# Optimization experiments

Hardware: AMD Instinct MI355X
Metric: run time of the kernel (lower is better)

## Reference

```python
import jax, jax.numpy as jnp
import numpy as np

B, S, DM, H, DK, DV, CUT = 2, 256, 512, 8, 64, 64, 16
LN_EPS = 1e-5


def get_con_vecs(seq, cutoff):
    # seq: (B, H, S, d). Faithful to torch: raw row-major reshape, NOT a transpose.
    b, h, s, d = seq.shape
    D = h * d
    flat = seq.reshape(b, s, D)                       # raw reinterpretation as in torch
    t = jnp.broadcast_to(flat[:, None], (b, s, s, D)) # (B, S_rep, S_orig, D)
    t = t.transpose(0, 3, 1, 2)                       # (B, D, S, S)
    up = jnp.triu(t)
    up = jnp.flip(up, axis=2)
    up = jnp.pad(up, ((0, 0), (0, 0), (1, 0), (0, 0)))[:, :, :-1, :]
    low = jnp.tril(t)
    low = jnp.flip(low, axis=2)
    mtx = jnp.concatenate([up, low], axis=-1)         # (B, D, S, 2S)
    mtx = mtx.transpose(0, 2, 3, 1)                   # (B, S, 2S, D)
    mtx = mtx.reshape(b, h, s, 2 * s, d)              # raw reinterpretation as in torch
    c = min(cutoff, s)
    return mtx[:, :, :, s - c:s + c, :]               # (B, H, S, 2c, d)


def setup_inputs():
    key = jax.random.key(0)
    ks = jax.random.split(key, 14)
    n = lambda k, shp, sc=0.02: jax.random.normal(k, shp, dtype=jnp.float32) * sc
    return {
        "Q": jax.random.normal(ks[0], (B, S, DM), dtype=jnp.float32),
        "K": jax.random.normal(ks[1], (B, S, DM), dtype=jnp.float32),
        "V": jax.random.normal(ks[2], (B, S, DM), dtype=jnp.float32),
        "attn_mask": jax.random.randint(ks[3], (B, S, S), 0, 2).astype(bool),
        "WQ": n(ks[4], (DM, H * DK)), "bQ": jnp.zeros((H * DK,), jnp.float32),
        "WK": n(ks[5], (DM, H * DK)), "bK": jnp.zeros((H * DK,), jnp.float32),
        "WV": n(ks[6], (DM, H * DV)), "bV": jnp.zeros((H * DV,), jnp.float32),
        "Wo": n(ks[7], (H * DV, DM)), "bo": jnp.zeros((DM,), jnp.float32),
        "gamma": jnp.ones((DM,), jnp.float32), "beta": jnp.zeros((DM,), jnp.float32),
    }


def reference(Q, K, V, attn_mask, WQ, bQ, WK, bK, WV, bV, Wo, bo, gamma, beta):
    b = Q.shape[0]
    q_s = (Q @ WQ + bQ).reshape(b, -1, H, DK).transpose(0, 2, 1, 3)  # (B,H,S,dk)
    k_s = (K @ WK + bK).reshape(b, -1, H, DK).transpose(0, 2, 1, 3)
    v_s = (V @ WV + bV).reshape(b, -1, H, DV).transpose(0, 2, 1, 3)  # unused in 'con' path (V := con(K))
    del v_s

    Qc = get_con_vecs(q_s, CUT)   # (B,H,S,2c,dk)
    Kc = get_con_vecs(k_s, CUT)
    Vc = Kc

    scores = jnp.einsum('bhqcd,bhkcd->bhqkc', Qc, Kc) / np.float32(np.sqrt(DK))
    mask = attn_mask[:, None, :, :, None]             # (B,1,S,S,1) -> broadcast over heads, 2c
    scores = jnp.where(mask, jnp.float32(-1e9), scores)
    attn = jax.nn.softmax(scores, axis=-1)            # softmax over the 2c context axis
    context = jnp.einsum('bhqkc,bhvcd->bhqd', attn, Vc)
    attn_out = attn.sum(axis=-1)                      # (B,H,S,S)

    ctx = context.transpose(0, 2, 1, 3).reshape(b, -1, H * DV)
    out = ctx @ Wo + bo
    y = out + Q
    mu = y.mean(axis=-1, keepdims=True)
    var = ((y - mu) ** 2).mean(axis=-1, keepdims=True)
    y_n = (y - mu) / jnp.sqrt(var + LN_EPS) * gamma + beta
    return (y_n, attn_out)
```

## Files before the change

### kernel.cpp

```cpp
#include <hip/hip_runtime.h>

#define LN_EPS 1e-5f


#define FMA4(a, s, v) { (a).x += (s)*(v).x; (a).y += (s)*(v).y; \
                        (a).z += (s)*(v).z; (a).w += (s)*(v).w; }

__device__ __forceinline__ bool sniff_mask_bytes(const unsigned int* m) {
    unsigned int acc = 0;
#pragma unroll
    for (int i = 0; i < 16; ++i) acc |= m[i];
    return acc > 1u;
}

__global__ __launch_bounds__(512) void kAo_proj_part(
    const float* __restrict__ Qin, const float* __restrict__ Kin,
    const float* __restrict__ WQ, const float* __restrict__ WK,
    float* __restrict__ Ppart)
{
    __shared__ float Xs[32][36];
    int bx = blockIdx.x;
    int mc = bx & 15, b = (bx >> 4) & 1, which = bx >> 5;
    int m0 = mc * 32;
    int t = threadIdx.x;

    const float* In = which ? Kin : Qin;
    const float* W  = which ? WK  : WQ;

#pragma unroll
    for (int i = 0; i < 2; ++i) {
        int idx = i * 512 + t;
        int fr = idx >> 5, mm = idx & 31;
        int cc = fr >> 3, cs = fr & 7;
        int srow = (cc < 2) ? (240 + 8 * cc + cs) : (8 * (cc - 2) + cs);
        Xs[mm][fr] = In[(b * 256 + srow) * 512 + m0 + mm];
    }
    __syncthreads();

    int h_i = t >> 6, g = t >> 7;
    int cc0 = (h_i & 1) * 2;
    float acc[16];
#pragma unroll
    for (int j = 0; j < 16; ++j) acc[j] = 0.f;

    const float* wp = W + t;
#pragma unroll 4
    for (int mm = 0; mm < 32; ++mm) {
        float w = wp[(m0 + mm) * 512];
        const float4* xp = (const float4*)&Xs[mm][cc0 * 8];
        float4 x0 = xp[0], x1 = xp[1], x2 = xp[2], x3 = xp[3];
        acc[0]  += x0.x * w; acc[1]  += x0.y * w; acc[2]  += x0.z * w; acc[3]  += x0.w * w;
        acc[4]  += x1.x * w; acc[5]  += x1.y * w; acc[6]  += x1.z * w; acc[7]  += x1.w * w;
        acc[8]  += x2.x * w; acc[9]  += x2.y * w; acc[10] += x2.z * w; acc[11] += x2.w * w;
        acc[12] += x3.x * w; acc[13] += x3.y * w; acc[14] += x3.z * w; acc[15] += x3.w * w;
    }

    int d = t & 63;
    int base = ((which * 2 + b) * 4 + g) * 4;
#pragma unroll
    for (int j = 0; j < 16; ++j) {
        int ccj = cc0 + (j >> 3), cs = j & 7;
        Ppart[mc * 32768 + (base + ccj) * 512 + cs * 64 + d] = acc[j];
    }
}

__global__ void kB_proj_red(const float* __restrict__ Ppart,
                            const float* __restrict__ bQ, const float* __restrict__ bK,
                            float* __restrict__ F) {
    int f = blockIdx.x * 256 + threadIdx.x;
    float acc = 0.f;
#pragma unroll
    for (int kc = 0; kc < 16; ++kc) acc += Ppart[kc * 32768 + f];
    int which = f >> 14, cc = (f >> 9) & 3, g = (f >> 11) & 3, d = f & 63;
    int n = (g * 2 + (cc >> 1)) * 64 + d;
    F[f] = acc + (which ? bK[n] : bQ[n]);
}

__global__ void kC_dtab_sfk(const float* __restrict__ F, float* __restrict__ Dt,
                            float* __restrict__ SFK) {
    int slot = blockIdx.x * 256 + threadIdx.x;
    if (slot < 8192) {
        int part = slot & 7, e = slot >> 3;
        int cs = e & 7, cc = (e >> 3) & 3, gk = (e >> 5) & 3,
            gq = (e >> 7) & 3, b = (e >> 9) & 1;
        const float* fq = F + ((b * 4 + gq) * 4 + cc) * 512 + cs * 64 + part * 8;
        const float* fk = F + (((2 + b) * 4 + gk) * 4 + cc) * 512 + cs * 64 + part * 8;
        float a = 0.f;
#pragma unroll
        for (int u = 0; u < 8; ++u) a += fq[u] * fk[u];
        a += __shfl_xor(a, 1);
        a += __shfl_xor(a, 2);
        a += __shfl_xor(a, 4);
        if (part == 0) Dt[e] = a * 0.125f;
    } else {
        int e = slot - 8192;
        int d = e & 63, c = (e >> 6) & 31, b = e >> 11;
        float a = 0.f;
#pragma unroll
        for (int gv = 0; gv < 4; ++gv)
            a += F[(((2 + b) * 4 + gv) * 4 + (c >> 3)) * 512 + (c & 7) * 64 + d];
        SFK[e] = 32.f * a;
    }
}

__global__ void kAttn(const float* __restrict__ Dt, const void* __restrict__ maskp,
                      const float* __restrict__ SFK, float* __restrict__ ctx,
                      float* __restrict__ attnp, int fill) {
    __shared__ float aws[4][32];
    int vb = blockIdx.x, t = threadIdx.x;
    if (fill) ((float4*)attnp)[vb * 256 + t] = make_float4(1.f, 1.f, 1.f, 1.f);
    int qb = vb & 63, h = (vb >> 6) & 7, b = vb >> 9;
    int wave = t >> 6, l = t & 63;
    int q = qb * 4 + wave;
    int half = l & 1, klo = l >> 1;
    int g_q = q & 3;
    int i_q = h * 32 + (q >> 3);
    bool up_q = (q & 4) == 0;
    int ak = klo & 3;
    bool up_k = (klo & 4) == 0;

    bool mbytes = sniff_mask_bytes((const unsigned int*)maskp);

    float sq[16];
    const float* Db = Dt + ((b * 4 + g_q) * 4 + ak) * 32 + half * 16;
#pragma unroll
    for (int j = 0; j < 16; ++j) {
        int cc = half * 2 + (j >> 3);
        int row = g_q * 64 + 30 + cc;
        bool vq = up_q ? (i_q >= 256 - row) : (i_q <= 255 - row);
        sq[j] = vq ? Db[j] : 0.f;
    }

    float A[16];
#pragma unroll
    for (int j = 0; j < 16; ++j) A[j] = 0.f;

    int qrow = (b * 256 + q) * 256;
    for (int r = 0; r < 8; ++r) {
        int k = r * 32 + klo;
        bool masked = mbytes ? (((const unsigned char*)maskp)[qrow + k] != 0)
                             : (((const int*)maskp)[qrow + k] != 0);
        if (masked) {
#pragma unroll
            for (int j = 0; j < 16; ++j) A[j] += 0.03125f;
            continue;
        }
        int i_k = h * 32 + (k >> 3);
        float s[16];
        float mx = -1e30f;
#pragma unroll
        for (int j = 0; j < 16; ++j) {
            int cc = half * 2 + (j >> 3);
            int row = ak * 64 + 30 + cc;
            bool vk = up_k ? (i_k >= 256 - row) : (i_k <= 255 - row);
            s[j] = vk ? sq[j] : 0.f;
            mx = fmaxf(mx, s[j]);
        }
        mx = fmaxf(mx, __shfl_xor(mx, 1));
        float den = 0.f;
#pragma unroll
        for (int j = 0; j < 16; ++j) { s[j] = __expf(s[j] - mx); den += s[j]; }
        den += __shfl_xor(den, 1);
        float inv = 1.f / den;
#pragma unroll
        for (int j = 0; j < 16; ++j) A[j] += s[j] * inv;
    }

#pragma unroll
    for (int off = 2; off < 64; off <<= 1) {
#pragma unroll
        for (int j = 0; j < 16; ++j) A[j] += __shfl_xor(A[j], off);
    }

    float* aw = aws[wave];
    if (l < 2) {
#pragma unroll
        for (int j = 0; j < 16; ++j) aw[l * 16 + j] = A[j];
    }
    float acc = 0.f;
    const float* S = SFK + b * 2048;
#pragma unroll
    for (int c = 0; c < 32; ++c) acc += aw[c] * S[c * 64 + l];
    ctx[(b * 256 + q) * 512 + h * 64 + l] = acc;
}

__global__ __launch_bounds__(512) void kG4LN(
    const float* __restrict__ ctx, const float* __restrict__ Wo,
    const float* __restrict__ bo, const float* __restrict__ Qin,
    const float* __restrict__ gamma, const float* __restrict__ beta,
    float* __restrict__ out)
{
    __shared__ float  Cl[4][512];
    __shared__ float4 red4[8][4][64];
    __shared__ float  red2[8][2];

    int t = threadIdx.x, r0 = blockIdx.x * 4;
    int w = t >> 6, l = t & 63;

    ((float4*)Cl)[t] = ((const float4*)&ctx[r0 * 512])[t];
    __syncthreads();

    const float4* WoV = (const float4*)Wo;
    const float4* pA = WoV + (size_t)(w * 64) * 128 + l;
    const float4* pB = pA + 64;
    float4 a0A = {0,0,0,0}, a1A = {0,0,0,0}, a2A = {0,0,0,0}, a3A = {0,0,0,0};
    float4 a0B = {0,0,0,0}, a1B = {0,0,0,0}, a2B = {0,0,0,0}, a3B = {0,0,0,0};
    int m0 = w * 64;
    float4 wA = pA[0], wB = pB[0];
#pragma unroll 4
    for (int mm = 0; mm < 63; ++mm) {
        float4 nA = pA[(mm + 1) * 128];
        float4 nB = pB[(mm + 1) * 128];
        float s0 = Cl[0][m0 + mm], s1 = Cl[1][m0 + mm];
        float s2 = Cl[2][m0 + mm], s3 = Cl[3][m0 + mm];
        FMA4(a0A, s0, wA); FMA4(a1A, s1, wA); FMA4(a2A, s2, wA); FMA4(a3A, s3, wA);
        FMA4(a0B, s0, wB); FMA4(a1B, s1, wB); FMA4(a2B, s2, wB); FMA4(a3B, s3, wB);
        wA = nA; wB = nB;
    }
    {
        float s0 = Cl[0][m0 + 63], s1 = Cl[1][m0 + 63];
        float s2 = Cl[2][m0 + 63], s3 = Cl[3][m0 + 63];
        FMA4(a0A, s0, wA); FMA4(a1A, s1, wA); FMA4(a2A, s2, wA); FMA4(a3A, s3, wA);
        FMA4(a0B, s0, wB); FMA4(a1B, s1, wB); FMA4(a2B, s2, wB); FMA4(a3B, s3, wB);
    }

    red4[w][0][l] = a0A; red4[w][1][l] = a1A; red4[w][2][l] = a2A; red4[w][3][l] = a3A;
    __syncthreads();
    if (t < 256) {
        int r = t >> 6, c4 = t & 63;
        float4 s = red4[0][r][c4];
#pragma unroll
        for (int w2 = 1; w2 < 8; ++w2) {
            float4 v = red4[w2][r][c4];
            s.x += v.x; s.y += v.y; s.z += v.z; s.w += v.w;
        }
        float4 bb = ((const float4*)bo)[c4];
        float4 qq = ((const float4*)Qin)[(r0 + r) * 128 + c4];
        s.x += bb.x + qq.x; s.y += bb.y + qq.y;
        s.z += bb.z + qq.z; s.w += bb.w + qq.w;
        *(float4*)&Cl[r][c4 * 4] = s;
    }
    __syncthreads();
    red4[w][0][l] = a0B; red4[w][1][l] = a1B; red4[w][2][l] = a2B; red4[w][3][l] = a3B;
    __syncthreads();
    if (t < 256) {
        int r = t >> 6, c4 = t & 63;
        float4 s = red4[0][r][c4];
#pragma unroll
        for (int w2 = 1; w2 < 8; ++w2) {
            float4 v = red4[w2][r][c4];
            s.x += v.x; s.y += v.y; s.z += v.z; s.w += v.w;
        }
        float4 bb = ((const float4*)bo)[64 + c4];
        float4 qq = ((const float4*)Qin)[(r0 + r) * 128 + 64 + c4];
        s.x += bb.x + qq.x; s.y += bb.y + qq.y;
        s.z += bb.z + qq.z; s.w += bb.w + qq.w;
        *(float4*)&Cl[r][256 + c4 * 4] = s;
    }
    __syncthreads();

    int r = t >> 7, c = t & 127;
    float v0 = Cl[r][c], v1 = Cl[r][c + 128], v2 = Cl[r][c + 256], v3 = Cl[r][c + 384];
    float s1 = v0 + v1 + v2 + v3;
    float s2 = v0 * v0 + v1 * v1 + v2 * v2 + v3 * v3;
#pragma unroll
    for (int off = 1; off < 64; off <<= 1) {
        s1 += __shfl_xor(s1, off);
        s2 += __shfl_xor(s2, off);
    }
    if (l == 0) { red2[w][0] = s1; red2[w][1] = s2; }
    __syncthreads();
    float tot1 = red2[2 * r][0] + red2[2 * r + 1][0];
    float tot2 = red2[2 * r][1] + red2[2 * r + 1][1];
    float mu = tot1 * (1.f / 512.f);
    float var = tot2 * (1.f / 512.f) - mu * mu;
    float rs = rsqrtf(var + LN_EPS);
    float* op = out + (r0 + r) * 512;
    op[c]       = (v0 - mu) * rs * gamma[c]       + beta[c];
    op[c + 128] = (v1 - mu) * rs * gamma[c + 128] + beta[c + 128];
    op[c + 256] = (v2 - mu) * rs * gamma[c + 256] + beta[c + 256];
    op[c + 384] = (v3 - mu) * rs * gamma[c + 384] + beta[c + 384];
}

__global__ void k5_fill(float* __restrict__ p, int n) {
    int i = (blockIdx.x * 256 + threadIdx.x) * 4;
    float4 one = make_float4(1.f, 1.f, 1.f, 1.f);
    for (; i < n; i += gridDim.x * 256 * 4) *(float4*)(p + i) = one;
}

extern "C" void kernel_launch(void* const* d_in, const int* in_sizes, int n_in,
                              void* d_out, int out_size, void* d_ws, size_t ws_size,
                              hipStream_t stream) {
    (void)in_sizes; (void)n_in; (void)out_size;
    const float* Qin  = (const float*)d_in[0];
    const float* Kin  = (const float*)d_in[1];
    const void*  mask = d_in[3];
    const float* WQ   = (const float*)d_in[4];
    const float* bQ   = (const float*)d_in[5];
    const float* WK   = (const float*)d_in[6];
    const float* bK   = (const float*)d_in[7];
    const float* Wo   = (const float*)d_in[10];
    const float* bo   = (const float*)d_in[11];
    const float* gamma= (const float*)d_in[12];
    const float* beta = (const float*)d_in[13];

    float* out   = (float*)d_out;
    float* attnp = out + 262144;

    const size_t NEED = 824320ull * sizeof(float);
    if (ws_size >= NEED) {
        float* ws    = (float*)d_ws;
        float* Ppart = ws;
        float* F     = ws + 524288;
        float* Dt    = ws + 557056;
        float* SFK   = ws + 558080;
        float* ctx   = ws + 562176;

        kAo_proj_part<<<dim3(64),  dim3(512), 0, stream>>>(Qin, Kin, WQ, WK, Ppart);
        kB_proj_red <<<dim3(128),  dim3(256), 0, stream>>>(Ppart, bQ, bK, F);
        kC_dtab_sfk <<<dim3(48),   dim3(256), 0, stream>>>(F, Dt, SFK);
        kAttn       <<<dim3(1024), dim3(256), 0, stream>>>(Dt, mask, SFK, ctx, attnp, 1);
        kG4LN       <<<dim3(128),  dim3(512), 0, stream>>>(ctx, Wo, bo, Qin, gamma, beta, out);
    } else {
        float* Ppart = attnp;
        float* F     = attnp + 524288;
        float* Dt    = attnp + 557056;
        float* SFK   = attnp + 558080;
        float* ctx   = attnp + 786432;

        kAo_proj_part<<<dim3(64),  dim3(512), 0, stream>>>(Qin, Kin, WQ, WK, Ppart);
        kB_proj_red <<<dim3(128),  dim3(256), 0, stream>>>(Ppart, bQ, bK, F);
        kC_dtab_sfk <<<dim3(48),   dim3(256), 0, stream>>>(F, Dt, SFK);
        kAttn       <<<dim3(1024), dim3(256), 0, stream>>>(Dt, mask, SFK, ctx, attnp, 0);
        kG4LN       <<<dim3(128),  dim3(512), 0, stream>>>(ctx, Wo, bo, Qin, gamma, beta, out);
        k5_fill     <<<dim3(256),  dim3(256), 0, stream>>>(attnp, 1048576);
    }
}
```

Before: 38.87 us.

## Replace split-K reduction with atomics and fuse score-table build into attention

The projection kernel now accumulates its split-K partial sums straight into F with atomicAdd, adding the bias from the first chunk only; a memset zeroes F before it runs. This removes the separate reduction kernel. The Dt and SFK tables are now rebuilt per block in shared memory inside the attention kernel, removing the table kernel and two launches. The price is heavy redundant recomputation and L2 reads across 1024 blocks, atomic contention, and a float summation order that is no longer deterministic.

```diff
diff --git a/kernel.cpp b/kernel.cpp
--- a/kernel.cpp
+++ b/kernel.cpp
@@ -13,10 +13,11 @@
     return acc > 1u;
 }
 
-__global__ __launch_bounds__(512) void kAo_proj_part(
+__global__ __launch_bounds__(512) void kAo_at(
     const float* __restrict__ Qin, const float* __restrict__ Kin,
-    const float* __restrict__ WQ, const float* __restrict__ WK,
-    float* __restrict__ Ppart)
+    const float* __restrict__ WQ, const float* __restrict__ bQ,
+    const float* __restrict__ WK, const float* __restrict__ bK,
+    float* __restrict__ F)
 {
     __shared__ float Xs[32][36];
     int bx = blockIdx.x;
@@ -55,61 +56,51 @@
         acc[12] += x3.x * w; acc[13] += x3.y * w; acc[14] += x3.z * w; acc[15] += x3.w * w;
     }
 
+    float bb = (mc == 0) ? (which ? bK[t] : bQ[t]) : 0.f;
     int d = t & 63;
     int base = ((which * 2 + b) * 4 + g) * 4;
 #pragma unroll
     for (int j = 0; j < 16; ++j) {
         int ccj = cc0 + (j >> 3), cs = j & 7;
-        Ppart[mc * 32768 + (base + ccj) * 512 + cs * 64 + d] = acc[j];
-    }
-}
-
-__global__ void kB_proj_red(const float* __restrict__ Ppart,
-                            const float* __restrict__ bQ, const float* __restrict__ bK,
-                            float* __restrict__ F) {
-    int f = blockIdx.x * 256 + threadIdx.x;
-    float acc = 0.f;
-#pragma unroll
-    for (int kc = 0; kc < 16; ++kc) acc += Ppart[kc * 32768 + f];
-    int which = f >> 14, cc = (f >> 9) & 3, g = (f >> 11) & 3, d = f & 63;
-    int n = (g * 2 + (cc >> 1)) * 64 + d;
-    F[f] = acc + (which ? bK[n] : bQ[n]);
-}
-
-__global__ void kC_dtab_sfk(const float* __restrict__ F, float* __restrict__ Dt,
-                            float* __restrict__ SFK) {
-    int slot = blockIdx.x * 256 + threadIdx.x;
-    if (slot < 8192) {
-        int part = slot & 7, e = slot >> 3;
-        int cs = e & 7, cc = (e >> 3) & 3, gk = (e >> 5) & 3,
-            gq = (e >> 7) & 3, b = (e >> 9) & 1;
-        const float* fq = F + ((b * 4 + gq) * 4 + cc) * 512 + cs * 64 + part * 8;
-        const float* fk = F + (((2 + b) * 4 + gk) * 4 + cc) * 512 + cs * 64 + part * 8;
-        float a = 0.f;
-#pragma unroll
-        for (int u = 0; u < 8; ++u) a += fq[u] * fk[u];
-        a += __shfl_xor(a, 1);
-        a += __shfl_xor(a, 2);
-        a += __shfl_xor(a, 4);
-        if (part == 0) Dt[e] = a * 0.125f;
-    } else {
-        int e = slot - 8192;
-        int d = e & 63, c = (e >> 6) & 31, b = e >> 11;
-        float a = 0.f;
-#pragma unroll
-        for (int gv = 0; gv < 4; ++gv)
-            a += F[(((2 + b) * 4 + gv) * 4 + (c >> 3)) * 512 + (c & 7) * 64 + d];
-        SFK[e] = 32.f * a;
-    }
-}
-
-__global__ void kAttn(const float* __restrict__ Dt, const void* __restrict__ maskp,
-                      const float* __restrict__ SFK, float* __restrict__ ctx,
-                      float* __restrict__ attnp, int fill) {
+        atomicAdd(&F[(base + ccj) * 512 + cs * 64 + d], acc[j] + bb);
+    }
+}
+
+__global__ void kAttnF(const float* __restrict__ F, const void* __restrict__ maskp,
+                       float* __restrict__ ctx, float* __restrict__ attnp, int fill) {
+    __shared__ float Dt_s[512];
+    __shared__ float SFK_s[2048];
     __shared__ float aws[4][32];
     int vb = blockIdx.x, t = threadIdx.x;
     if (fill) ((float4*)attnp)[vb * 256 + t] = make_float4(1.f, 1.f, 1.f, 1.f);
     int qb = vb & 63, h = (vb >> 6) & 7, b = vb >> 9;
+
+#pragma unroll
+    for (int rep = 0; rep < 2; ++rep) {
+        int eb = rep * 256 + t;
+        int gq = eb >> 7, ak = (eb >> 5) & 3, cc = (eb >> 3) & 3, cs = eb & 7;
+        const float4* fq = (const float4*)(F + ((b * 4 + gq) * 4 + cc) * 512 + cs * 64);
+        const float4* fk = (const float4*)(F + (((2 + b) * 4 + ak) * 4 + cc) * 512 + cs * 64);
+        float a = 0.f;
+#pragma unroll
+        for (int u = 0; u < 16; ++u) {
+            float4 x = fq[u], y = fk[u];
+            a += x.x * y.x + x.y * y.y + x.z * y.z + x.w * y.w;
+        }
+        Dt_s[eb] = a * 0.125f;
+    }
+#pragma unroll
+    for (int rep = 0; rep < 8; ++rep) {
+        int es = rep * 256 + t;
+        int c = es >> 6, d = es & 63;
+        float a = 0.f;
+#pragma unroll
+        for (int gv = 0; gv < 4; ++gv)
+            a += F[(((2 + b) * 4 + gv) * 4 + (c >> 3)) * 512 + (c & 7) * 64 + d];
+        SFK_s[es] = 32.f * a;
+    }
+    __syncthreads();
+
     int wave = t >> 6, l = t & 63;
     int q = qb * 4 + wave;
     int half = l & 1, klo = l >> 1;
@@ -122,7 +113,7 @@
     bool mbytes = sniff_mask_bytes((const unsigned int*)maskp);
 
     float sq[16];
-    const float* Db = Dt + ((b * 4 + g_q) * 4 + ak) * 32 + half * 16;
+    const float* Db = Dt_s + (g_q * 4 + ak) * 32 + half * 16;
 #pragma unroll
     for (int j = 0; j < 16; ++j) {
         int cc = half * 2 + (j >> 3);
@@ -178,9 +169,8 @@
         for (int j = 0; j < 16; ++j) aw[l * 16 + j] = A[j];
     }
     float acc = 0.f;
-    const float* S = SFK + b * 2048;
-#pragma unroll
-    for (int c = 0; c < 32; ++c) acc += aw[c] * S[c * 64 + l];
+#pragma unroll
+    for (int c = 0; c < 32; ++c) acc += aw[c] * SFK_s[c * 64 + l];
     ctx[(b * 256 + q) * 512 + h * 64 + l] = acc;
 }
 
@@ -307,32 +297,22 @@
     float* out   = (float*)d_out;
     float* attnp = out + 262144;
 
-    const size_t NEED = 824320ull * sizeof(float);
+    const size_t NEED = 294912ull * sizeof(float);
+    int fill;
+    float *F, *ctx;
     if (ws_size >= NEED) {
-        float* ws    = (float*)d_ws;
-        float* Ppart = ws;
-        float* F     = ws + 524288;
-        float* Dt    = ws + 557056;
-        float* SFK   = ws + 558080;
-        float* ctx   = ws + 562176;
-
-        kAo_proj_part<<<dim3(64),  dim3(512), 0, stream>>>(Qin, Kin, WQ, WK, Ppart);
-        kB_proj_red <<<dim3(128),  dim3(256), 0, stream>>>(Ppart, bQ, bK, F);
-        kC_dtab_sfk <<<dim3(48),   dim3(256), 0, stream>>>(F, Dt, SFK);
-        kAttn       <<<dim3(1024), dim3(256), 0, stream>>>(Dt, mask, SFK, ctx, attnp, 1);
-        kG4LN       <<<dim3(128),  dim3(512), 0, stream>>>(ctx, Wo, bo, Qin, gamma, beta, out);
+        F   = (float*)d_ws;
+        ctx = (float*)d_ws + 32768;
+        fill = 1;
     } else {
-        float* Ppart = attnp;
-        float* F     = attnp + 524288;
-        float* Dt    = attnp + 557056;
-        float* SFK   = attnp + 558080;
-        float* ctx   = attnp + 786432;
-
-        kAo_proj_part<<<dim3(64),  dim3(512), 0, stream>>>(Qin, Kin, WQ, WK, Ppart);
-        kB_proj_red <<<dim3(128),  dim3(256), 0, stream>>>(Ppart, bQ, bK, F);
-        kC_dtab_sfk <<<dim3(48),   dim3(256), 0, stream>>>(F, Dt, SFK);
-        kAttn       <<<dim3(1024), dim3(256), 0, stream>>>(Dt, mask, SFK, ctx, attnp, 0);
-        kG4LN       <<<dim3(128),  dim3(512), 0, stream>>>(ctx, Wo, bo, Qin, gamma, beta, out);
-        k5_fill     <<<dim3(256),  dim3(256), 0, stream>>>(attnp, 1048576);
-    }
-}
+        F   = attnp + 524288;
+        ctx = attnp + 786432;
+        fill = 0;
+    }
+
+    hipMemsetAsync(F, 0, 32768 * sizeof(float), stream);
+    kAo_at <<<dim3(64),   dim3(512), 0, stream>>>(Qin, Kin, WQ, bQ, WK, bK, F);
+    kAttnF <<<dim3(1024), dim3(256), 0, stream>>>(F, mask, ctx, attnp, fill);
+    kG4LN  <<<dim3(128),  dim3(512), 0, stream>>>(ctx, Wo, bo, Qin, gamma, beta, out);
+    if (!fill) k5_fill<<<dim3(256), dim3(256), 0, stream>>>(attnp, 1048576);
+}
```

Result: slower. 78.72 us (+102.5%).

## Replace split-K partial buffer with atomic accumulation and widen output projection block

Applied to the files above, without the earlier changes.

The projection kernel now adds its split-K partial results straight into a zeroed feature buffer with atomicAdd, folding in the bias from the first chunk. This removes the separate reduction kernel and the large partial-sum buffer, at the cost of a memset launch and atomic contention from 16 chunks per element. The output projection plus LayerNorm kernel now runs 1024 threads per block, with each wave computing one column half instead of two, which raises parallelism but adds an extra barrier. Float atomics also make the summation order nondeterministic.

```diff
diff --git a/kernel.cpp b/kernel.cpp
--- a/kernel.cpp
+++ b/kernel.cpp
@@ -13,10 +13,11 @@
     return acc > 1u;
 }
 
-__global__ __launch_bounds__(512) void kAo_proj_part(
+__global__ __launch_bounds__(512) void kAo_at(
     const float* __restrict__ Qin, const float* __restrict__ Kin,
-    const float* __restrict__ WQ, const float* __restrict__ WK,
-    float* __restrict__ Ppart)
+    const float* __restrict__ WQ, const float* __restrict__ bQ,
+    const float* __restrict__ WK, const float* __restrict__ bK,
+    float* __restrict__ F)
 {
     __shared__ float Xs[32][36];
     int bx = blockIdx.x;
@@ -55,25 +56,14 @@
         acc[12] += x3.x * w; acc[13] += x3.y * w; acc[14] += x3.z * w; acc[15] += x3.w * w;
     }
 
+    float bb = (mc == 0) ? (which ? bK[t] : bQ[t]) : 0.f;
     int d = t & 63;
     int base = ((which * 2 + b) * 4 + g) * 4;
 #pragma unroll
     for (int j = 0; j < 16; ++j) {
         int ccj = cc0 + (j >> 3), cs = j & 7;
-        Ppart[mc * 32768 + (base + ccj) * 512 + cs * 64 + d] = acc[j];
-    }
-}
-
-__global__ void kB_proj_red(const float* __restrict__ Ppart,
-                            const float* __restrict__ bQ, const float* __restrict__ bK,
-                            float* __restrict__ F) {
-    int f = blockIdx.x * 256 + threadIdx.x;
-    float acc = 0.f;
-#pragma unroll
-    for (int kc = 0; kc < 16; ++kc) acc += Ppart[kc * 32768 + f];
-    int which = f >> 14, cc = (f >> 9) & 3, g = (f >> 11) & 3, d = f & 63;
-    int n = (g * 2 + (cc >> 1)) * 64 + d;
-    F[f] = acc + (which ? bK[n] : bQ[n]);
+        atomicAdd(&F[(base + ccj) * 512 + cs * 64 + d], acc[j] + bb);
+    }
 }
 
 __global__ void kC_dtab_sfk(const float* __restrict__ F, float* __restrict__ Dt,
@@ -184,7 +174,7 @@
     ctx[(b * 256 + q) * 512 + h * 64 + l] = acc;
 }
 
-__global__ __launch_bounds__(512) void kG4LN(
+__global__ __launch_bounds__(1024) void kG4LN2(
     const float* __restrict__ ctx, const float* __restrict__ Wo,
     const float* __restrict__ bo, const float* __restrict__ Qin,
     const float* __restrict__ gamma, const float* __restrict__ beta,
@@ -192,46 +182,43 @@
 {
     __shared__ float  Cl[4][512];
     __shared__ float4 red4[8][4][64];
-    __shared__ float  red2[8][2];
+    __shared__ float  red2[4][4][2];
 
     int t = threadIdx.x, r0 = blockIdx.x * 4;
     int w = t >> 6, l = t & 63;
-
-    ((float4*)Cl)[t] = ((const float4*)&ctx[r0 * 512])[t];
-    __syncthreads();
-
-    const float4* WoV = (const float4*)Wo;
-    const float4* pA = WoV + (size_t)(w * 64) * 128 + l;
-    const float4* pB = pA + 64;
-    float4 a0A = {0,0,0,0}, a1A = {0,0,0,0}, a2A = {0,0,0,0}, a3A = {0,0,0,0};
-    float4 a0B = {0,0,0,0}, a1B = {0,0,0,0}, a2B = {0,0,0,0}, a3B = {0,0,0,0};
-    int m0 = w * 64;
-    float4 wA = pA[0], wB = pB[0];
+    int mc = w >> 1, h2 = w & 1;
+    int m0 = mc * 64;
+
+    if (t < 512) ((float4*)Cl)[t] = ((const float4*)&ctx[r0 * 512])[t];
+    __syncthreads();
+
+    const float4* p = (const float4*)Wo + (size_t)m0 * 128 + h2 * 64 + l;
+    float4 a0 = {0,0,0,0}, a1 = {0,0,0,0}, a2 = {0,0,0,0}, a3 = {0,0,0,0};
+    float4 wv = p[0];
 #pragma unroll 4
     for (int mm = 0; mm < 63; ++mm) {
-        float4 nA = pA[(mm + 1) * 128];
-        float4 nB = pB[(mm + 1) * 128];
+        float4 nx = p[(mm + 1) * 128];
         float s0 = Cl[0][m0 + mm], s1 = Cl[1][m0 + mm];
         float s2 = Cl[2][m0 + mm], s3 = Cl[3][m0 + mm];
-        FMA4(a0A, s0, wA); FMA4(a1A, s1, wA); FMA4(a2A, s2, wA); FMA4(a3A, s3, wA);
-        FMA4(a0B, s0, wB); FMA4(a1B, s1, wB); FMA4(a2B, s2, wB); FMA4(a3B, s3, wB);
-        wA = nA; wB = nB;
+        FMA4(a0, s0, wv); FMA4(a1, s1, wv); FMA4(a2, s2, wv); FMA4(a3, s3, wv);
+        wv = nx;
     }
     {
         float s0 = Cl[0][m0 + 63], s1 = Cl[1][m0 + 63];
         float s2 = Cl[2][m0 + 63], s3 = Cl[3][m0 + 63];
-        FMA4(a0A, s0, wA); FMA4(a1A, s1, wA); FMA4(a2A, s2, wA); FMA4(a3A, s3, wA);
-        FMA4(a0B, s0, wB); FMA4(a1B, s1, wB); FMA4(a2B, s2, wB); FMA4(a3B, s3, wB);
-    }
-
-    red4[w][0][l] = a0A; red4[w][1][l] = a1A; red4[w][2][l] = a2A; red4[w][3][l] = a3A;
+        FMA4(a0, s0, wv); FMA4(a1, s1, wv); FMA4(a2, s2, wv); FMA4(a3, s3, wv);
+    }
+    __syncthreads();
+
+    if (h2 == 0) { red4[mc][0][l] = a0; red4[mc][1][l] = a1;
+                   red4[mc][2][l] = a2; red4[mc][3][l] = a3; }
     __syncthreads();
     if (t < 256) {
         int r = t >> 6, c4 = t & 63;
         float4 s = red4[0][r][c4];
 #pragma unroll
-        for (int w2 = 1; w2 < 8; ++w2) {
-            float4 v = red4[w2][r][c4];
+        for (int u = 1; u < 8; ++u) {
+            float4 v = red4[u][r][c4];
             s.x += v.x; s.y += v.y; s.z += v.z; s.w += v.w;
         }
         float4 bb = ((const float4*)bo)[c4];
@@ -241,14 +228,15 @@
         *(float4*)&Cl[r][c4 * 4] = s;
     }
     __syncthreads();
-    red4[w][0][l] = a0B; red4[w][1][l] = a1B; red4[w][2][l] = a2B; red4[w][3][l] = a3B;
+    if (h2 == 1) { red4[mc][0][l] = a0; red4[mc][1][l] = a1;
+                   red4[mc][2][l] = a2; red4[mc][3][l] = a3; }
     __syncthreads();
     if (t < 256) {
         int r = t >> 6, c4 = t & 63;
         float4 s = red4[0][r][c4];
 #pragma unroll
-        for (int w2 = 1; w2 < 8; ++w2) {
-            float4 v = red4[w2][r][c4];
+        for (int u = 1; u < 8; ++u) {
+            float4 v = red4[u][r][c4];
             s.x += v.x; s.y += v.y; s.z += v.z; s.w += v.w;
         }
         float4 bb = ((const float4*)bo)[64 + c4];
@@ -259,27 +247,24 @@
     }
     __syncthreads();
 
-    int r = t >> 7, c = t & 127;
-    float v0 = Cl[r][c], v1 = Cl[r][c + 128], v2 = Cl[r][c + 256], v3 = Cl[r][c + 384];
-    float s1 = v0 + v1 + v2 + v3;
-    float s2 = v0 * v0 + v1 * v1 + v2 * v2 + v3 * v3;
+    int r = t >> 8, cc = t & 255;
+    float y0 = Cl[r][cc], y1 = Cl[r][cc + 256];
+    float s1 = y0 + y1, s2 = y0 * y0 + y1 * y1;
 #pragma unroll
     for (int off = 1; off < 64; off <<= 1) {
         s1 += __shfl_xor(s1, off);
         s2 += __shfl_xor(s2, off);
     }
-    if (l == 0) { red2[w][0] = s1; red2[w][1] = s2; }
-    __syncthreads();
-    float tot1 = red2[2 * r][0] + red2[2 * r + 1][0];
-    float tot2 = red2[2 * r][1] + red2[2 * r + 1][1];
+    if (l == 0) { red2[r][w & 3][0] = s1; red2[r][w & 3][1] = s2; }
+    __syncthreads();
+    float tot1 = red2[r][0][0] + red2[r][1][0] + red2[r][2][0] + red2[r][3][0];
+    float tot2 = red2[r][0][1] + red2[r][1][1] + red2[r][2][1] + red2[r][3][1];
     float mu = tot1 * (1.f / 512.f);
     float var = tot2 * (1.f / 512.f) - mu * mu;
     float rs = rsqrtf(var + LN_EPS);
     float* op = out + (r0 + r) * 512;
-    op[c]       = (v0 - mu) * rs * gamma[c]       + beta[c];
-    op[c + 128] = (v1 - mu) * rs * gamma[c + 128] + beta[c + 128];
-    op[c + 256] = (v2 - mu) * rs * gamma[c + 256] + beta[c + 256];
-    op[c + 384] = (v3 - mu) * rs * gamma[c + 384] + beta[c + 384];
+    op[cc]       = (y0 - mu) * rs * gamma[cc]       + beta[cc];
+    op[cc + 256] = (y1 - mu) * rs * gamma[cc + 256] + beta[cc + 256];
 }
 
 __global__ void k5_fill(float* __restrict__ p, int n) {
@@ -307,32 +292,28 @@
     float* out   = (float*)d_out;
     float* attnp = out + 262144;
 
-    const size_t NEED = 824320ull * sizeof(float);
+    const size_t NEED = 300032ull * sizeof(float);
+    int fill;
+    float *F, *Dt, *SFK, *ctx;
     if (ws_size >= NEED) {
-        float* ws    = (float*)d_ws;
-        float* Ppart = ws;
-        float* F     = ws + 524288;
-        float* Dt    = ws + 557056;
-        float* SFK   = ws + 558080;
-        float* ctx   = ws + 562176;
-
-        kAo_proj_part<<<dim3(64),  dim3(512), 0, stream>>>(Qin, Kin, WQ, WK, Ppart);
-        kB_proj_red <<<dim3(128),  dim3(256), 0, stream>>>(Ppart, bQ, bK, F);
-        kC_dtab_sfk <<<dim3(48),   dim3(256), 0, stream>>>(F, Dt, SFK);
-        kAttn       <<<dim3(1024), dim3(256), 0, stream>>>(Dt, mask, SFK, ctx, attnp, 1);
-        kG4LN       <<<dim3(128),  dim3(512), 0, stream>>>(ctx, Wo, bo, Qin, gamma, beta, out);
+        float* ws = (float*)d_ws;
+        F   = ws;
+        Dt  = ws + 32768;
+        SFK = ws + 33792;
+        ctx = ws + 37888;
+        fill = 1;
     } else {
-        float* Ppart = attnp;
-        float* F     = attnp + 524288;
-        float* Dt    = attnp + 557056;
-        float* SFK   = attnp + 558080;
-        float* ctx   = attnp + 786432;
-
-        kAo_proj_part<<<dim3(64),  dim3(512), 0, stream>>>(Qin, Kin, WQ, WK, Ppart);
-        kB_proj_red <<<dim3(128),  dim3(256), 0, stream>>>(Ppart, bQ, bK, F);
-        kC_dtab_sfk <<<dim3(48),   dim3(256), 0, stream>>>(F, Dt, SFK);
-        kAttn       <<<dim3(1024), dim3(256), 0, stream>>>(Dt, mask, SFK, ctx, attnp, 0);
-        kG4LN       <<<dim3(128),  dim3(512), 0, stream>>>(ctx, Wo, bo, Qin, gamma, beta, out);
-        k5_fill     <<<dim3(256),  dim3(256), 0, stream>>>(attnp, 1048576);
-    }
-}
+        F   = attnp + 524288;
+        Dt  = attnp + 557056;
+        SFK = attnp + 558080;
+        ctx = attnp + 786432;
+        fill = 0;
+    }
+
+    hipMemsetAsync(F, 0, 32768 * sizeof(float), stream);
+    kAo_at     <<<dim3(64),   dim3(512),  0, stream>>>(Qin, Kin, WQ, bQ, WK, bK, F);
+    kC_dtab_sfk<<<dim3(48),   dim3(256),  0, stream>>>(F, Dt, SFK);
+    kAttn      <<<dim3(1024), dim3(256),  0, stream>>>(Dt, mask, SFK, ctx, attnp, fill);
+    kG4LN2     <<<dim3(128),  dim3(1024), 0, stream>>>(ctx, Wo, bo, Qin, gamma, beta, out);
+    if (!fill) k5_fill<<<dim3(256), dim3(256), 0, stream>>>(attnp, 1048576);
+}
```

After: 44.50 us. 1.14x slower.
